# Optimization experiments

Hardware: AMD Instinct MI355X
Metric: run time of the kernel (lower is better)

The kernel has to match this reference:

```python
import jax, jax.numpy as jnp
import numpy as np

N = 30000   # nodes
E = 150000  # edges per graph
IN = 512
HID = 512
OUT = 256
G = 3


def setup_inputs() -> dict:
    key = jax.random.key(0)
    ks = jax.random.split(key, 16)
    inp = {"x": jax.random.normal(ks[0], (N, IN), jnp.float32)}
    for i in range(G):
        inp[f"edges{i}"] = jax.random.randint(ks[1 + i], (2, E), 0, N)
        inp[f"W{i}"] = jax.random.normal(ks[4 + i], (IN, HID), jnp.float32) / np.sqrt(IN)
        inp[f"b{i}"] = jnp.zeros((HID,), jnp.float32)
    inp["alphas"] = jnp.ones((G,), jnp.float32)
    inp["W_lin"] = jax.random.normal(ks[8], (HID * G, OUT), jnp.float32) / np.sqrt(HID * G)
    inp["b_lin"] = jnp.zeros((OUT,), jnp.float32)
    return inp


def graph_conv(edges, x, W, b):
    # DGL GraphConv, norm='both': out = D_in^{-1/2} A D_out^{-1/2} (X W) + b
    src, dst = edges[0], edges[1]
    ones = jnp.ones(edges.shape[1], x.dtype)
    deg_out = jnp.clip(jax.ops.segment_sum(ones, src, num_segments=N), 1.0)  # out-degree of src nodes
    deg_in = jnp.clip(jax.ops.segment_sum(ones, dst, num_segments=N), 1.0)   # in-degree of dst nodes
    h = (x * jax.lax.rsqrt(deg_out)[:, None]) @ W        # [N, HID] mult-W-first (in_dim >= hid_dim)
    agg = jax.ops.segment_sum(h[src], dst, num_segments=N)  # SpMM via gather + scatter-add
    return agg * jax.lax.rsqrt(deg_in)[:, None] + b


def reference(x, edges0, edges1, edges2, W0, W1, W2, b0, b1, b2, alphas, W_lin, b_lin):
    a = jax.nn.softmax(alphas)  # softmax over the n_graphs axis
    branches = [(edges0, W0, b0), (edges1, W1, b1), (edges2, W2, b2)]
    hs = [jnp.tanh(a[i] * graph_conv(e, x, W, b)) for i, (e, W, b) in enumerate(branches)]
    h = jnp.concatenate(hs, axis=1)  # [N, G*HID]; dropout(p=0) is identity
    return h @ W_lin + b_lin
```

## Files before the change

### kernel.cpp

```cpp
#include <hip/hip_runtime.h>

#define NN 30000
#define NE 150000
#define KIN 512
#define KHID 512
#define KOUT 256
#define NG 3
#define KCAT (KHID*NG)
#define MTILES ((NN + 127) / 128)
#define MT64   ((NN + 63) / 64)
#define NCHUNK 30

typedef __attribute__((ext_vector_type(8))) __bf16 bf16x8;
typedef __attribute__((ext_vector_type(4))) float  f32x4;
typedef __attribute__((ext_vector_type(8))) unsigned short u16x8;

__device__ __forceinline__ unsigned short f2bf(float f) {
    unsigned u = __float_as_uint(f);
    u = (u + 0x7FFFu + ((u >> 16) & 1u)) >> 16;
    return (unsigned short)u;
}
__device__ __forceinline__ float bf2f(unsigned short u) {
    return __uint_as_float((unsigned)u << 16);
}
__device__ __forceinline__ float fast_tanh(float x) {
    float e = __expf(2.f * x);
    return 1.f - __fdividef(2.f, e + 1.f);
}
__device__ __forceinline__ void gl_lds16(const void* g, void* l) {
    __builtin_amdgcn_global_load_lds(
        (const __attribute__((address_space(1))) void*)g,
        (__attribute__((address_space(3))) void*)l, 16, 0, 0);
}

__global__ void k_count(const int* __restrict__ e0, const int* __restrict__ e1,
                        const int* __restrict__ e2, int* cnt_out, int* cnt_in) {
    int idx = blockIdx.x * 256 + threadIdx.x;
    if (idx >= NG * NE) return;
    int g = idx / NE, e = idx - g * NE;
    const int* ed = (g == 0) ? e0 : ((g == 1) ? e1 : e2);
    atomicAdd(&cnt_out[g * NN + ed[e]], 1);
    atomicAdd(&cnt_in [g * NN + ed[NE + e]], 1);
}

__global__ void k_rs(const int* cnt_out, const int* cnt_in, float* rs_out, float* rs_in) {
    int idx = blockIdx.x * 256 + threadIdx.x;
    if (idx >= NG * NN) return;
    int co = cnt_out[idx]; if (co < 1) co = 1;
    int ci = cnt_in [idx]; if (ci < 1) ci = 1;
    rs_out[idx] = rsqrtf((float)co);
    rs_in [idx] = rsqrtf((float)ci);
}

__global__ __launch_bounds__(256) void k_scan1(const int* __restrict__ cnt_in,
                                               int* __restrict__ csum) {
    int g = blockIdx.y, c = blockIdx.x;
    const int* cc = cnt_in + g * NN;
    int i = c * 1024 + threadIdx.x * 4;
    int4 v = {0, 0, 0, 0};
    if (i + 3 < NN) v = *(const int4*)(cc + i);
    else {
        if (i     < NN) v.x = cc[i];
        if (i + 1 < NN) v.y = cc[i + 1];
        if (i + 2 < NN) v.z = cc[i + 2];
        if (i + 3 < NN) v.w = cc[i + 3];
    }
    int s = v.x + v.y + v.z + v.w;
    #pragma unroll
    for (int o = 32; o > 0; o >>= 1) s += __shfl_down(s, o, 64);
    __shared__ int ws[4];
    if ((threadIdx.x & 63) == 0) ws[threadIdx.x >> 6] = s;
    __syncthreads();
    if (threadIdx.x == 0) csum[g * 32 + c] = ws[0] + ws[1] + ws[2] + ws[3];
}

__global__ void k_scan2(int* __restrict__ csum) {
    int g = threadIdx.x >> 6, lane = threadIdx.x & 63;
    if (g >= NG) return;
    int v = (lane < NCHUNK) ? csum[g * 32 + lane] : 0;
    int inc = v;
    #pragma unroll
    for (int o = 1; o < 32; o <<= 1) {
        int n = __shfl_up(inc, o, 64);
        if (lane >= o) inc += n;
    }
    if (lane < NCHUNK) csum[g * 32 + lane] = inc - v;
}

__global__ __launch_bounds__(256) void k_scan3(const int* __restrict__ cnt_in,
        const int* __restrict__ csum, int* __restrict__ row_off) {
    int g = blockIdx.y, c = blockIdx.x;
    const int* cc = cnt_in + g * NN;
    int* ro = row_off + g * (NN + 1);
    int tid = threadIdx.x, lane = tid & 63, w = tid >> 6;
    int i = c * 1024 + tid * 4;
    int4 v = {0, 0, 0, 0};
    if (i + 3 < NN) v = *(const int4*)(cc + i);
    else {
        if (i     < NN) v.x = cc[i];
        if (i + 1 < NN) v.y = cc[i + 1];
        if (i + 2 < NN) v.z = cc[i + 2];
        if (i + 3 < NN) v.w = cc[i + 3];
    }
    int s = v.x + v.y + v.z + v.w;
    int inc = s;
    #pragma unroll
    for (int o = 1; o < 64; o <<= 1) {
        int n = __shfl_up(inc, o, 64);
        if (lane >= o) inc += n;
    }
    __shared__ int ws[4];
    if (lane == 63) ws[w] = inc;
    __syncthreads();
    int base = csum[g * 32 + c];
    for (int k = 0; k < w; k++) base += ws[k];
    int excl = base + inc - s;
    if (i     < NN) ro[i]     = excl;
    if (i + 1 < NN) ro[i + 1] = excl + v.x;
    if (i + 2 < NN) ro[i + 2] = excl + v.x + v.y;
    if (i + 3 < NN) ro[i + 3] = excl + v.x + v.y + v.z;
    if (c == 0 && tid == 0) ro[NN] = NE;
}

__global__ void k_fill(const int* __restrict__ e0, const int* __restrict__ e1,
                       const int* __restrict__ e2, const int* __restrict__ row_off,
                       int* cursor, int* __restrict__ csr) {
    int idx = blockIdx.x * 256 + threadIdx.x;
    if (idx >= NG * NE) return;
    int g = idx / NE, e = idx - g * NE;
    const int* ed = (g == 0) ? e0 : ((g == 1) ? e1 : e2);
    int s = ed[e], d = ed[NE + e];
    int pos = atomicAdd(&cursor[g * NN + d], 1);
    csr[g * NE + row_off[g * (NN + 1) + d] + pos] = s;
}

__global__ void k_misc(const float* __restrict__ alphas,
                       const float* __restrict__ b0, const float* __restrict__ b1,
                       const float* __restrict__ b2, float* __restrict__ aptr,
                       float* __restrict__ bcat) {
    int idx = blockIdx.x * 256 + threadIdx.x;
    if (idx < NG * KHID) {
        int g = idx >> 9;
        const float* b = (g == 0) ? b0 : ((g == 1) ? b1 : b2);
        bcat[idx] = b[idx & 511];
    }
    if (idx == 0) {
        float m = fmaxf(alphas[0], fmaxf(alphas[1], alphas[2]));
        float ex0 = expf(alphas[0] - m), ex1 = expf(alphas[1] - m), ex2 = expf(alphas[2] - m);
        float s = ex0 + ex1 + ex2;
        aptr[0] = ex0 / s; aptr[1] = ex1 / s; aptr[2] = ex2 / s;
    }
}

__global__ __launch_bounds__(256) void k_wt(const float* __restrict__ W0,
        const float* __restrict__ W1, const float* __restrict__ W2,
        const float* __restrict__ Wlin,
        unsigned short* __restrict__ Wt, unsigned short* __restrict__ Wlt) {
    __shared__ float Ls[32][33];
    int bid = blockIdx.x;
    const float* src; unsigned short* dst; int ncols, kdim, k0, n0;
    if (bid < NG * 256) {
        int g = bid >> 8, t = bid & 255;
        int kt = t >> 4, nt = t & 15;
        src = (g == 0) ? W0 : ((g == 1) ? W1 : W2);
        dst = Wt + (size_t)g * KIN * KHID;
        ncols = KHID; kdim = KIN; k0 = kt * 32; n0 = nt * 32;
    } else {
        int t = bid - NG * 256;
        int kt = t % 48, nt = t / 48;
        src = Wlin; dst = Wlt; ncols = KOUT; kdim = KCAT; k0 = kt * 32; n0 = nt * 32;
    }
    int tid = threadIdx.x;
    int r = tid >> 3, c4 = (tid & 7) * 4;
    float4 v = *(const float4*)(src + (size_t)(k0 + r) * ncols + n0 + c4);
    Ls[r][c4 + 0] = v.x; Ls[r][c4 + 1] = v.y; Ls[r][c4 + 2] = v.z; Ls[r][c4 + 3] = v.w;
    __syncthreads();
    int nr = tid >> 3, kc = (tid & 7) * 4;
    ushort4 o;
    o.x = f2bf(Ls[kc + 0][nr]); o.y = f2bf(Ls[kc + 1][nr]);
    o.z = f2bf(Ls[kc + 2][nr]); o.w = f2bf(Ls[kc + 3][nr]);
    *(ushort4*)(dst + (size_t)(n0 + nr) * kdim + k0 + kc) = o;
}

__global__ void k_xbf(const float* __restrict__ x, unsigned short* __restrict__ xb) {
    size_t i = ((size_t)blockIdx.x * 256 + threadIdx.x) * 8;
    float4 v0 = *(const float4*)(x + i);
    float4 v1 = *(const float4*)(x + i + 4);
    uint4 pk;
    pk.x = (unsigned)f2bf(v0.x) | ((unsigned)f2bf(v0.y) << 16);
    pk.y = (unsigned)f2bf(v0.z) | ((unsigned)f2bf(v0.w) << 16);
    pk.z = (unsigned)f2bf(v1.x) | ((unsigned)f2bf(v1.y) << 16);
    pk.w = (unsigned)f2bf(v1.z) | ((unsigned)f2bf(v1.w) << 16);
    *(uint4*)(xb + i) = pk;
}

__global__ __launch_bounds__(256) void k_agg_bf(const unsigned short* __restrict__ xb,
        const int* __restrict__ csr, const int* __restrict__ row_off,
        const float* __restrict__ rs_out, const float* __restrict__ rs_in,
        unsigned short* __restrict__ y, size_t ystride, int gbase) {
    int g    = gbase + blockIdx.z;
    int d    = blockIdx.x * 4 + (threadIdx.x >> 6);
    int lane = threadIdx.x & 63;
    int beg = row_off[g * (NN + 1) + d];
    int end = row_off[g * (NN + 1) + d + 1];
    const int* cs = csr + g * NE;
    const float* rso = rs_out + g * NN;
    float a0=0,a1=0,a2=0,a3=0,a4=0,a5=0,a6=0,a7=0;
    const unsigned short* xbl = xb + lane * 8;
    int e = beg;
    for (; e + 3 < end; e += 4) {
        int s0 = cs[e], s1 = cs[e+1], s2 = cs[e+2], s3 = cs[e+3];
        float w0 = rso[s0], w1 = rso[s1], w2 = rso[s2], w3 = rso[s3];
        u16x8 v0 = *(const u16x8*)(xbl + (size_t)s0 * KIN);
        u16x8 v1 = *(const u16x8*)(xbl + (size_t)s1 * KIN);
        u16x8 v2 = *(const u16x8*)(xbl + (size_t)s2 * KIN);
        u16x8 v3 = *(const u16x8*)(xbl + (size_t)s3 * KIN);
        a0 += w0*bf2f(v0[0]) + w1*bf2f(v1[0]) + w2*bf2f(v2[0]) + w3*bf2f(v3[0]);
        a1 += w0*bf2f(v0[1]) + w1*bf2f(v1[1]) + w2*bf2f(v2[1]) + w3*bf2f(v3[1]);
        a2 += w0*bf2f(v0[2]) + w1*bf2f(v1[2]) + w2*bf2f(v2[2]) + w3*bf2f(v3[2]);
        a3 += w0*bf2f(v0[3]) + w1*bf2f(v1[3]) + w2*bf2f(v2[3]) + w3*bf2f(v3[3]);
        a4 += w0*bf2f(v0[4]) + w1*bf2f(v1[4]) + w2*bf2f(v2[4]) + w3*bf2f(v3[4]);
        a5 += w0*bf2f(v0[5]) + w1*bf2f(v1[5]) + w2*bf2f(v2[5]) + w3*bf2f(v3[5]);
        a6 += w0*bf2f(v0[6]) + w1*bf2f(v1[6]) + w2*bf2f(v2[6]) + w3*bf2f(v3[6]);
        a7 += w0*bf2f(v0[7]) + w1*bf2f(v1[7]) + w2*bf2f(v2[7]) + w3*bf2f(v3[7]);
    }
    for (; e < end; e++) {
        int s0 = cs[e];
        float w0 = rso[s0];
        u16x8 v0 = *(const u16x8*)(xbl + (size_t)s0 * KIN);
        a0 += w0 * bf2f(v0[0]); a1 += w0 * bf2f(v0[1]);
        a2 += w0 * bf2f(v0[2]); a3 += w0 * bf2f(v0[3]);
        a4 += w0 * bf2f(v0[4]); a5 += w0 * bf2f(v0[5]);
        a6 += w0 * bf2f(v0[6]); a7 += w0 * bf2f(v0[7]);
    }
    float ri = rs_in[g * NN + d];
    uint4 pk;
    pk.x = (unsigned)f2bf(a0 * ri) | ((unsigned)f2bf(a1 * ri) << 16);
    pk.y = (unsigned)f2bf(a2 * ri) | ((unsigned)f2bf(a3 * ri) << 16);
    pk.z = (unsigned)f2bf(a4 * ri) | ((unsigned)f2bf(a5 * ri) << 16);
    pk.w = (unsigned)f2bf(a6 * ri) | ((unsigned)f2bf(a7 * ri) << 16);
    *(uint4*)(y + (size_t)g * ystride + (size_t)d * KIN + lane * 8) = pk;
}

__global__ __launch_bounds__(256) void k_agg_f32(const float* __restrict__ x,
        const int* __restrict__ csr, const int* __restrict__ row_off,
        const float* __restrict__ rs_out, const float* __restrict__ rs_in,
        unsigned short* __restrict__ y, int g) {
    int d    = blockIdx.x * 4 + (threadIdx.x >> 6);
    int lane = threadIdx.x & 63;
    int beg = row_off[g * (NN + 1) + d];
    int end = row_off[g * (NN + 1) + d + 1];
    const int* cs = csr + g * NE;
    float a0=0,a1=0,a2=0,a3=0,a4=0,a5=0,a6=0,a7=0;
    const float* xb = x + lane * 8;
    for (int e = beg; e < end; e++) {
        int s = cs[e];
        float wsc = rs_out[g * NN + s];
        const float4* xr = (const float4*)(xb + (size_t)s * KIN);
        float4 v0 = xr[0], v1 = xr[1];
        a0 += wsc * v0.x; a1 += wsc * v0.y; a2 += wsc * v0.z; a3 += wsc * v0.w;
        a4 += wsc * v1.x; a5 += wsc * v1.y; a6 += wsc * v1.z; a7 += wsc * v1.w;
    }
    float ri = rs_in[g * NN + d];
    uint4 pk;
    pk.x = (unsigned)f2bf(a0 * ri) | ((unsigned)f2bf(a1 * ri) << 16);
    pk.y = (unsigned)f2bf(a2 * ri) | ((unsigned)f2bf(a3 * ri) << 16);
    pk.z = (unsigned)f2bf(a4 * ri) | ((unsigned)f2bf(a5 * ri) << 16);
    pk.w = (unsigned)f2bf(a6 * ri) | ((unsigned)f2bf(a7 * ri) << 16);
    *(uint4*)(y + (size_t)d * KIN + lane * 8) = pk;
}

template<int KDIM, int BM, int BN, bool TANH>
__global__ __launch_bounds__(256) void k_gemm(const unsigned short* __restrict__ A,
        size_t agstride, const unsigned short* __restrict__ Bt,
        const float* __restrict__ bias, const float* __restrict__ aptr, int gbase,
        unsigned short* __restrict__ Tout, float* __restrict__ Fout) {
    constexpr int NITER = KDIM / 32;
    constexpr int ACH = BM * 4 / 256;
    constexpr int BCH = BN * 4 / 256;
    constexpr int MQ = BM / 64;
    __shared__ __align__(16) unsigned short As[2][BM * 32];
    __shared__ __align__(16) unsigned short Bs[2][BN * 32];
    int g = gbase + blockIdx.z;
    const unsigned short* Ab = A + (size_t)g * agstride;
    const unsigned short* Bb = (TANH ? (Bt + (size_t)g * KIN * KHID) : Bt);
    const float* bb = TANH ? (bias + g * KHID) : bias;
    int m0 = blockIdx.y * BM;
    int n0 = blockIdx.x * BN;
    int tid = threadIdx.x, lane = tid & 63, w = tid >> 6;
    int mq = w % MQ, nq = w / MQ;

    f32x4 acc[4][4];
    #pragma unroll
    for (int i = 0; i < 4; i++)
        #pragma unroll
        for (int j = 0; j < 4; j++) acc[i][j] = (f32x4){0.f, 0.f, 0.f, 0.f};

    const unsigned short* Ag[ACH];
    unsigned short* Al[ACH];
    #pragma unroll
    for (int j = 0; j < ACH; j++) {
        int c = tid + 256 * j;
        int r = c >> 2, q = (c & 3) ^ ((c >> 3) & 3);
        int grow = m0 + r; if (grow >= NN) grow = NN - 1;
        Ag[j] = Ab + (size_t)grow * KDIM + q * 8;
        Al[j] = (unsigned short*)&As[0][c * 8];
    }
    const unsigned short* Bg[BCH];
    unsigned short* Bl[BCH];
    #pragma unroll
    for (int j = 0; j < BCH; j++) {
        int c = tid + 256 * j;
        int r = c >> 2, q = (c & 3) ^ ((c >> 3) & 3);
        Bg[j] = Bb + (size_t)(n0 + r) * KDIM + q * 8;
        Bl[j] = (unsigned short*)&Bs[0][c * 8];
    }
    constexpr int ABUF = BM * 32, BBUF = BN * 32;

    auto stage = [&](int buf, int k0) {
        #pragma unroll
        for (int j = 0; j < ACH; j++) gl_lds16(Ag[j] + k0, Al[j] + buf * ABUF);
        #pragma unroll
        for (int j = 0; j < BCH; j++) gl_lds16(Bg[j] + k0, Bl[j] + buf * BBUF);
    };

    int kqs = (((lane >> 4) ^ ((lane >> 1) & 3))) * 8;
    int arow = mq * 64 + (lane & 15);
    int nrow = nq * 64 + (lane & 15);

    stage(0, 0);
    for (int it = 0; it < NITER; it++) {
        __syncthreads();
        if (it + 1 < NITER) stage((it + 1) & 1, (it + 1) * 32);
        const unsigned short* Alb = As[it & 1];
        const unsigned short* Blb = Bs[it & 1];
        bf16x8 af[4], bfr[4];
        #pragma unroll
        for (int mi = 0; mi < 4; mi++) af[mi] = *(const bf16x8*)&Alb[(arow + mi * 16) * 32 + kqs];
        #pragma unroll
        for (int ni = 0; ni < 4; ni++) bfr[ni] = *(const bf16x8*)&Blb[(nrow + ni * 16) * 32 + kqs];
        #pragma unroll
        for (int mi = 0; mi < 4; mi++)
            #pragma unroll
            for (int ni = 0; ni < 4; ni++)
                acc[mi][ni] = __builtin_amdgcn_mfma_f32_16x16x32_bf16(af[mi], bfr[ni], acc[mi][ni], 0, 0, 0);
    }

    float ascale = TANH ? aptr[g] : 0.f;
    int rb = mq * 64 + (lane >> 4) * 4;
    #pragma unroll
    for (int mi = 0; mi < 4; mi++) {
        #pragma unroll
        for (int r = 0; r < 4; r++) {
            int row = m0 + rb + mi * 16 + r;
            if (row < NN) {
                #pragma unroll
                for (int ni = 0; ni < 4; ni++) {
                    int col = n0 + nq * 64 + ni * 16 + (lane & 15);
                    float v = acc[mi][ni][r] + bb[col];
                    if (TANH) {
                        Tout[(size_t)row * KCAT + g * KHID + col] = f2bf(fast_tanh(ascale * v));
                    } else {
                        Fout[(size_t)row * KOUT + col] = v;
                    }
                }
            }
        }
    }
}

extern "C" void kernel_launch(void* const* d_in, const int* in_sizes, int n_in,
                              void* d_out, int out_size, void* d_ws, size_t ws_size,
                              hipStream_t stream) {
    const float* x      = (const float*)d_in[0];
    const int*   e0     = (const int*)  d_in[1];
    const float* W0     = (const float*)d_in[2];
    const float* b0     = (const float*)d_in[3];
    const int*   e1     = (const int*)  d_in[4];
    const float* W1     = (const float*)d_in[5];
    const float* b1     = (const float*)d_in[6];
    const int*   e2     = (const int*)  d_in[7];
    const float* W2     = (const float*)d_in[8];
    const float* b2     = (const float*)d_in[9];
    const float* alphas = (const float*)d_in[10];
    const float* Wlin   = (const float*)d_in[11];
    const float* blin   = (const float*)d_in[12];
    float* out = (float*)d_out;

    char* ws = (char*)d_ws;
    size_t off = 0;
    auto alloc = [&](size_t bytes) -> void* {
        void* p = ws + off;
        off = (off + bytes + 255) & ~(size_t)255;
        return p;
    };
    int*   cnt_out = (int*)  alloc((size_t)NG * NN * 4);
    int*   cnt_in  = (int*)  alloc((size_t)NG * NN * 4);
    int*   cursor  = (int*)  alloc((size_t)NG * NN * 4);
    int*   row_off = (int*)  alloc((size_t)NG * (NN + 1) * 4);
    int*   csr     = (int*)  alloc((size_t)NG * NE * 4);
    int*   csum    = (int*)  alloc((size_t)NG * 32 * 4);
    float* rs_out  = (float*)alloc((size_t)NG * NN * 4);
    float* rs_in   = (float*)alloc((size_t)NG * NN * 4);
    float* aptr    = (float*)alloc(16);
    float* bcat    = (float*)alloc((size_t)NG * KHID * 4);
    unsigned short* Wt  = (unsigned short*)alloc((size_t)NG * KIN * KHID * 2);
    unsigned short* Wlt = (unsigned short*)alloc((size_t)KCAT * KOUT * 2);

    const size_t SZ_Y1 = (size_t)NN * KIN * 2;
    const size_t SZ_T  = (size_t)NN * KCAT * 2;
    size_t remaining = (ws_size > off) ? (ws_size - off) : 0;
    int mode;
    if      (remaining >= 3 * SZ_Y1 + SZ_T + 8192)          mode = 2;
    else if (remaining >= SZ_Y1 + SZ_Y1 + SZ_T + 8192)      mode = 1;
    else                                                    mode = 0;

    unsigned short *y, *xb, *t;
    if (mode == 2) {
        y  = (unsigned short*)alloc(3 * SZ_Y1);
        t  = (unsigned short*)alloc(SZ_T);
        xb = t;
    } else if (mode == 1) {
        y  = (unsigned short*)alloc(SZ_Y1);
        xb = (unsigned short*)alloc(SZ_Y1);
        t  = (unsigned short*)alloc(SZ_T);
    } else {
        y  = (unsigned short*)alloc(SZ_Y1);
        xb = nullptr;
        t  = (unsigned short*)alloc(SZ_T);
    }

    hipMemsetAsync(cnt_out, 0, (size_t)((char*)cursor - (char*)cnt_out) + (size_t)NG * NN * 4, stream);

    k_count<<<(NG * NE + 255) / 256, 256, 0, stream>>>(e0, e1, e2, cnt_out, cnt_in);
    k_rs<<<(NG * NN + 255) / 256, 256, 0, stream>>>(cnt_out, cnt_in, rs_out, rs_in);
    k_scan1<<<dim3(NCHUNK, NG), 256, 0, stream>>>(cnt_in, csum);
    k_scan2<<<1, 192, 0, stream>>>(csum);
    k_scan3<<<dim3(NCHUNK, NG), 256, 0, stream>>>(cnt_in, csum, row_off);
    k_fill<<<(NG * NE + 255) / 256, 256, 0, stream>>>(e0, e1, e2, row_off, cursor, csr);
    k_misc<<<(NG * KHID + 255) / 256, 256, 0, stream>>>(alphas, b0, b1, b2, aptr, bcat);
    k_wt<<<NG * 256 + 384, 256, 0, stream>>>(W0, W1, W2, Wlin, Wt, Wlt);

    if (mode >= 1) {
        k_xbf<<<NN * KIN / (256 * 8), 256, 0, stream>>>(x, xb);
    }

    if (mode == 2) {
        k_agg_bf<<<dim3(NN / 4, 1, NG), 256, 0, stream>>>(
            xb, csr, row_off, rs_out, rs_in, y, (size_t)NN * KIN, 0);
        k_gemm<KIN, 128, 128, true><<<dim3(KHID / 128, MTILES, NG), 256, 0, stream>>>(
            y, (size_t)NN * KIN, Wt, bcat, aptr, 0, t, nullptr);
    } else {
        for (int g = 0; g < NG; g++) {
            if (mode == 1)
                k_agg_bf<<<dim3(NN / 4, 1, 1), 256, 0, stream>>>(
                    xb, csr, row_off, rs_out, rs_in, y, 0, g);
            else
                k_agg_f32<<<NN / 4, 256, 0, stream>>>(x, csr, row_off, rs_out, rs_in, y, g);
            k_gemm<KIN, 128, 128, true><<<dim3(KHID / 128, MTILES, 1), 256, 0, stream>>>(
                y, 0, Wt, bcat, aptr, g, t, nullptr);
        }
    }
    k_gemm<KCAT, 64, 256, false><<<dim3(1, MT64, 1), 256, 0, stream>>>(
        t, 0, Wlt, blin, nullptr, 0, nullptr, out);
}
```

Baseline: 405.5 us.

## Load GEMM B operand directly from global into registers, bypassing LDS

The GEMM kernel now stages only the A tile through LDS. Each wave loads its B fragments straight from global memory into registers, double-buffered one k-step ahead. The warp layout becomes a fixed 2x2 grid with per-wave tiles of BM/2 x BN/2. The final linear GEMM changes from a 64x256 tile to 64x128 with two column blocks. This removes B LDS traffic and the associated barrier pressure, at the cost of uncoalesced-ish 16-byte global loads for B that rely on cache reuse across blocks.

```diff
diff --git a/kernel.cpp b/kernel.cpp
--- a/kernel.cpp
+++ b/kernel.cpp
@@ -276,11 +276,11 @@
         const float* __restrict__ bias, const float* __restrict__ aptr, int gbase,
         unsigned short* __restrict__ Tout, float* __restrict__ Fout) {
     constexpr int NITER = KDIM / 32;
+    constexpr int MI = BM / 32;
+    constexpr int NI = BN / 32;
     constexpr int ACH = BM * 4 / 256;
-    constexpr int BCH = BN * 4 / 256;
-    constexpr int MQ = BM / 64;
-    __shared__ __align__(16) unsigned short As[2][BM * 32];
-    __shared__ __align__(16) unsigned short Bs[2][BN * 32];
+    constexpr int ABUF = BM * 32;
+    __shared__ __align__(16) unsigned short As[2][ABUF];
     int g = gbase + blockIdx.z;
     const unsigned short* Ab = A + (size_t)g * agstride;
     const unsigned short* Bb = (TANH ? (Bt + (size_t)g * KIN * KHID) : Bt);
@@ -288,13 +288,13 @@
     int m0 = blockIdx.y * BM;
     int n0 = blockIdx.x * BN;
     int tid = threadIdx.x, lane = tid & 63, w = tid >> 6;
-    int mq = w % MQ, nq = w / MQ;
-
-    f32x4 acc[4][4];
-    #pragma unroll
-    for (int i = 0; i < 4; i++)
-        #pragma unroll
-        for (int j = 0; j < 4; j++) acc[i][j] = (f32x4){0.f, 0.f, 0.f, 0.f};
+    int mq = w & 1, nq = w >> 1;
+
+    f32x4 acc[MI][NI];
+    #pragma unroll
+    for (int i = 0; i < MI; i++)
+        #pragma unroll
+        for (int j = 0; j < NI; j++) acc[i][j] = (f32x4){0.f, 0.f, 0.f, 0.f};
 
     const unsigned short* Ag[ACH];
     unsigned short* Al[ACH];
@@ -306,57 +306,55 @@
         Ag[j] = Ab + (size_t)grow * KDIM + q * 8;
         Al[j] = (unsigned short*)&As[0][c * 8];
     }
-    const unsigned short* Bg[BCH];
-    unsigned short* Bl[BCH];
-    #pragma unroll
-    for (int j = 0; j < BCH; j++) {
-        int c = tid + 256 * j;
-        int r = c >> 2, q = (c & 3) ^ ((c >> 3) & 3);
-        Bg[j] = Bb + (size_t)(n0 + r) * KDIM + q * 8;
-        Bl[j] = (unsigned short*)&Bs[0][c * 8];
-    }
-    constexpr int ABUF = BM * 32, BBUF = BN * 32;
-
     auto stage = [&](int buf, int k0) {
         #pragma unroll
         for (int j = 0; j < ACH; j++) gl_lds16(Ag[j] + k0, Al[j] + buf * ABUF);
-        #pragma unroll
-        for (int j = 0; j < BCH; j++) gl_lds16(Bg[j] + k0, Bl[j] + buf * BBUF);
     };
 
-    int kqs = (((lane >> 4) ^ ((lane >> 1) & 3))) * 8;
-    int arow = mq * 64 + (lane & 15);
-    int nrow = nq * 64 + (lane & 15);
-
+    const unsigned short* Bp[NI];
+    #pragma unroll
+    for (int ni = 0; ni < NI; ni++)
+        Bp[ni] = Bb + (size_t)(n0 + nq * (BN / 2) + ni * 16 + (lane & 15)) * KDIM + (lane >> 4) * 8;
+
+    int kqs = ((lane >> 4) ^ ((lane >> 1) & 3)) * 8;
+    int arow = mq * (BM / 2) + (lane & 15);
+
+    bf16x8 bc[NI], bn2[NI];
+    #pragma unroll
+    for (int ni = 0; ni < NI; ni++) bc[ni] = *(const bf16x8*)Bp[ni];
     stage(0, 0);
+
     for (int it = 0; it < NITER; it++) {
         __syncthreads();
-        if (it + 1 < NITER) stage((it + 1) & 1, (it + 1) * 32);
+        if (it + 1 < NITER) {
+            stage((it + 1) & 1, (it + 1) * 32);
+            #pragma unroll
+            for (int ni = 0; ni < NI; ni++) bn2[ni] = *(const bf16x8*)(Bp[ni] + (it + 1) * 32);
+        }
         const unsigned short* Alb = As[it & 1];
-        const unsigned short* Blb = Bs[it & 1];
-        bf16x8 af[4], bfr[4];
-        #pragma unroll
-        for (int mi = 0; mi < 4; mi++) af[mi] = *(const bf16x8*)&Alb[(arow + mi * 16) * 32 + kqs];
-        #pragma unroll
-        for (int ni = 0; ni < 4; ni++) bfr[ni] = *(const bf16x8*)&Blb[(nrow + ni * 16) * 32 + kqs];
-        #pragma unroll
-        for (int mi = 0; mi < 4; mi++)
+        bf16x8 af[MI];
+        #pragma unroll
+        for (int mi = 0; mi < MI; mi++) af[mi] = *(const bf16x8*)&Alb[(arow + mi * 16) * 32 + kqs];
+        #pragma unroll
+        for (int mi = 0; mi < MI; mi++)
             #pragma unroll
-            for (int ni = 0; ni < 4; ni++)
-                acc[mi][ni] = __builtin_amdgcn_mfma_f32_16x16x32_bf16(af[mi], bfr[ni], acc[mi][ni], 0, 0, 0);
+            for (int ni = 0; ni < NI; ni++)
+                acc[mi][ni] = __builtin_amdgcn_mfma_f32_16x16x32_bf16(af[mi], bc[ni], acc[mi][ni], 0, 0, 0);
+        #pragma unroll
+        for (int ni = 0; ni < NI; ni++) bc[ni] = bn2[ni];
     }
 
     float ascale = TANH ? aptr[g] : 0.f;
-    int rb = mq * 64 + (lane >> 4) * 4;
-    #pragma unroll
-    for (int mi = 0; mi < 4; mi++) {
+    int rb = mq * (BM / 2) + (lane >> 4) * 4;
+    #pragma unroll
+    for (int mi = 0; mi < MI; mi++) {
         #pragma unroll
         for (int r = 0; r < 4; r++) {
             int row = m0 + rb + mi * 16 + r;
             if (row < NN) {
                 #pragma unroll
-                for (int ni = 0; ni < 4; ni++) {
-                    int col = n0 + nq * 64 + ni * 16 + (lane & 15);
+                for (int ni = 0; ni < NI; ni++) {
+                    int col = n0 + nq * (BN / 2) + ni * 16 + (lane & 15);
                     float v = acc[mi][ni][r] + bb[col];
                     if (TANH) {
                         Tout[(size_t)row * KCAT + g * KHID + col] = f2bf(fast_tanh(ascale * v));
@@ -461,6 +459,6 @@
                 y, 0, Wt, bcat, aptr, g, t, nullptr);
         }
     }
-    k_gemm<KCAT, 64, 256, false><<<dim3(1, MT64, 1), 256, 0, stream>>>(
+    k_gemm<KCAT, 64, 128, false><<<dim3(KOUT / 128, MT64, 1), 256, 0, stream>>>(
         t, 0, Wlt, blin, nullptr, 0, nullptr, out);
 }
```

New measurement: 500.3 us. 1.23x slower.
